# Optimization experiments

Measured on AMD Instinct MI355X. Metric: run time of the kernel, lower is better.

The kernel has to match this reference:

```python
import jax, jax.numpy as jnp
import numpy as np

HEAD_SIZE = 32


def setup_inputs() -> dict:
    key = jax.random.key(0)
    ks = jax.random.split(key, 9)
    B, N, M = 2, 512, 512
    Dq = Dk = Dv = 128
    De = 64
    H, O, OUT = 8, HEAD_SIZE, 128
    s = 0.05  # keep logits tame
    return {
        "query": jax.random.normal(ks[0], (B, N, Dq), jnp.float32),
        "key": jax.random.normal(ks[1], (B, M, Dk), jnp.float32),
        "value": jax.random.normal(ks[2], (B, M, Dv), jnp.float32),
        "edge": jax.random.normal(ks[3], (B, N, M, De), jnp.float32),
        "query_kernel": jax.random.normal(ks[4], (H, Dq, O), jnp.float32) * s,
        "key_kernel": jax.random.normal(ks[5], (H, Dk + De, O), jnp.float32) * s,
        "value_kernel": jax.random.normal(ks[6], (H, Dv, O), jnp.float32) * s,
        "projection_kernel": jax.random.normal(ks[7], (H, O, OUT), jnp.float32) * s,
        "projection_bias": jnp.zeros((OUT,), jnp.float32),
    }


def reference(query, key, value, edge, query_kernel, key_kernel,
              value_kernel, projection_kernel, projection_bias):
    # Edge-conditioned keys: concat broadcast key [B,1,M,Dk] with edge [B,N,M,De]
    B, N, _ = query.shape
    M = key.shape[-2]
    key_rep = jnp.broadcast_to(key[..., None, :, :], (B, N, M, key.shape[-1]))
    key_cat = jnp.concatenate([key_rep, edge], axis=-1)           # [B,N,M,Dk+De]
    k = jnp.einsum('bnmi,hio->bnmho', key_cat, key_kernel)        # [B,N,M,H,O]
    q = jnp.einsum('bni,hio->bnho', query, query_kernel)
    q = q / jnp.sqrt(jnp.asarray(HEAD_SIZE, q.dtype))
    v = jnp.einsum('bmi,hio->bmho', value, value_kernel)
    logits = jnp.einsum('bnho,bnmho->bhnm', q, k)                 # [B,H,N,M]
    attn = jax.nn.softmax(logits, axis=-1)
    mh = jnp.einsum('bhnm,bmho->bnho', attn, v)                   # [B,N,H,O]
    out = jnp.einsum('bnhi,hio->bno', mh, projection_kernel)
    out = out + projection_bias
    return out
```

## Files before the change

kernel.cpp:

```cpp
#include <hip/hip_runtime.h>
#include <hip/hip_bf16.h>

#define B_   2
#define N_   512
#define M_   512
#define D_   128
#define DE_  64
#define H_   8
#define O_   32
#define OUT_ 128
#define DKE_ 192
#define MP_  516

typedef unsigned short u16;
typedef unsigned int   u32;
typedef short bf16x8 __attribute__((ext_vector_type(8)));
typedef float floatx4 __attribute__((ext_vector_type(4)));

__device__ __forceinline__ u32 pk2bf(float a, float b) {
    __hip_bfloat162 h = __float22bfloat162_rn(make_float2(a, b));
    return *reinterpret_cast<u32*>(&h);
}
__device__ __forceinline__ u16 f2bf(float a) {
    __hip_bfloat16 h = __float2bfloat16(a);
    return *reinterpret_cast<u16*>(&h);
}
__device__ __forceinline__ float bf2f(u16 x) {
    return __uint_as_float(((u32)x) << 16);
}
__device__ __forceinline__ bf16x8 cvt8(const float4 a, const float4 b) {
    union { u32 u[4]; bf16x8 v; } r;
    r.u[0] = pk2bf(a.x, a.y); r.u[1] = pk2bf(a.z, a.w);
    r.u[2] = pk2bf(b.x, b.y); r.u[3] = pk2bf(b.z, b.w);
    return r.v;
}

__global__ __launch_bounds__(256) void k_proj(
    const float* __restrict__ query, const float* __restrict__ Wq,
    const float* __restrict__ Wk,
    const float* __restrict__ value, const float* __restrict__ Wv,
    u16* __restrict__ qE, u16* __restrict__ vvT)
{
    const int t = threadIdx.x;
    __shared__ float Xs[8][D_];
    __shared__ float qh[8][H_ * O_];

    if (blockIdx.x < 128) {
        const int r0 = blockIdx.x * 8;
        reinterpret_cast<float4*>(&Xs[0][0])[t] =
            reinterpret_cast<const float4*>(query + (size_t)r0 * D_)[t];
        __syncthreads();
        {
            float acc[8] = {0,0,0,0,0,0,0,0};
            const float* wcol = Wq + (t >> 5) * (D_ * O_) + (t & 31);
            for (int k = 0; k < D_; k += 4) {
                const float w0 = wcol[(k+0) * O_];
                const float w1 = wcol[(k+1) * O_];
                const float w2 = wcol[(k+2) * O_];
                const float w3 = wcol[(k+3) * O_];
#pragma unroll
                for (int r = 0; r < 8; ++r) {
                    const float4 x = *reinterpret_cast<const float4*>(&Xs[r][k]);
                    acc[r] += x.x * w0 + x.y * w1 + x.z * w2 + x.w * w3;
                }
            }
#pragma unroll
            for (int r = 0; r < 8; ++r) qh[r][t] = acc[r] * 0.17677669529663687f;
        }
        __syncthreads();

        for (int s = 0; s < 6; ++s) {
            const int hj = t + 256 * s;
            const int h  = hj / DKE_;
            float w[O_];
#pragma unroll
            for (int i = 0; i < O_ / 4; ++i) {
                const float4 x = reinterpret_cast<const float4*>(Wk + (size_t)hj * O_)[i];
                w[4*i] = x.x; w[4*i+1] = x.y; w[4*i+2] = x.z; w[4*i+3] = x.w;
            }
#pragma unroll
            for (int r = 0; r < 8; ++r) {
                const float* qrow = &qh[r][h * O_];
                float a = 0.f;
#pragma unroll
                for (int i = 0; i < O_ / 4; ++i) {
                    const float4 qx = *reinterpret_cast<const float4*>(qrow + 4*i);
                    a += qx.x * w[4*i] + qx.y * w[4*i+1] + qx.z * w[4*i+2] + qx.w * w[4*i+3];
                }
                qE[(size_t)(r0 + r) * (H_ * DKE_) + hj] = f2bf(a);
            }
        }
    } else {
        const int r0 = (blockIdx.x - 128) * 8;
        reinterpret_cast<float4*>(&Xs[0][0])[t] =
            reinterpret_cast<const float4*>(value + (size_t)r0 * D_)[t];
        __syncthreads();

        float acc[8] = {0,0,0,0,0,0,0,0};
        const float* wcol = Wv + (t >> 5) * (D_ * O_) + (t & 31);
        for (int k = 0; k < D_; k += 4) {
            const float w0 = wcol[(k+0) * O_];
            const float w1 = wcol[(k+1) * O_];
            const float w2 = wcol[(k+2) * O_];
            const float w3 = wcol[(k+3) * O_];
#pragma unroll
            for (int r = 0; r < 8; ++r) {
                const float4 x = *reinterpret_cast<const float4*>(&Xs[r][k]);
                acc[r] += x.x * w0 + x.y * w1 + x.z * w2 + x.w * w3;
            }
        }
        const int bb = r0 >> 9, m0 = r0 & 511;
        union { u32 u[4]; uint4 q; } pk;
        pk.u[0] = pk2bf(acc[0], acc[1]);
        pk.u[1] = pk2bf(acc[2], acc[3]);
        pk.u[2] = pk2bf(acc[4], acc[5]);
        pk.u[3] = pk2bf(acc[6], acc[7]);
        *reinterpret_cast<uint4*>(vvT + (size_t)bb * 256 * M_ + (size_t)t * M_ + m0) = pk.q;
    }
}

__global__ __launch_bounds__(256, 4) void k_attn(
    const float* __restrict__ key, const float* __restrict__ edge,
    const u16* __restrict__ qE, const u16* __restrict__ vvT,
    const float* __restrict__ Wp, const float* __restrict__ bias,
    float* __restrict__ out)
{
    const int idx  = blockIdx.x;
    const int b    = idx >> 9;
    const int t    = threadIdx.x;
    const int lane = t & 63;
    const int wv   = t >> 6;

    __shared__ __attribute__((aligned(16))) float attn_s[H_][MP_];
    __shared__ float mh_s[H_ * O_];
    __shared__ float part_s[2][OUT_];

    const int br = lane & 15;
    const int q  = lane >> 4;

    bf16x8 afr[6];
    if (br < 8) {
        const u16* ab = qE + (size_t)idx * (H_ * DKE_) + br * DKE_;
#pragma unroll
        for (int kk = 0; kk < 6; ++kk)
            afr[kk] = *reinterpret_cast<const bf16x8*>(ab + kk * 32 + q * 8);
    } else {
#pragma unroll
        for (int kk = 0; kk < 6; ++kk) afr[kk] = bf16x8{0,0,0,0,0,0,0,0};
    }

    const float* keyb = key  + (size_t)b   * M_ * D_;
    const float* eb   = edge + (size_t)idx * M_ * DE_;

    for (int it = 0; it < 8; ++it) {
        const int tl = it * 4 + wv;
        const int m  = tl * 16 + br;
        const float* kr = keyb + (size_t)m * D_  + q * 8;
        const float* er = eb   + (size_t)m * DE_ + q * 8;
        float4 kf[8], ef[4];
#pragma unroll
        for (int kk = 0; kk < 4; ++kk) {
            kf[2*kk]   = *reinterpret_cast<const float4*>(kr + kk * 32);
            kf[2*kk+1] = *reinterpret_cast<const float4*>(kr + kk * 32 + 4);
        }
#pragma unroll
        for (int kk = 0; kk < 2; ++kk) {
            ef[2*kk]   = *reinterpret_cast<const float4*>(er + kk * 32);
            ef[2*kk+1] = *reinterpret_cast<const float4*>(er + kk * 32 + 4);
        }
        floatx4 acc = {0.f, 0.f, 0.f, 0.f};
#pragma unroll
        for (int kk = 0; kk < 4; ++kk)
            acc = __builtin_amdgcn_mfma_f32_16x16x32_bf16(afr[kk], cvt8(kf[2*kk], kf[2*kk+1]), acc, 0, 0, 0);
#pragma unroll
        for (int kk = 0; kk < 2; ++kk)
            acc = __builtin_amdgcn_mfma_f32_16x16x32_bf16(afr[4+kk], cvt8(ef[2*kk], ef[2*kk+1]), acc, 0, 0, 0);
        if (q < 2) {
#pragma unroll
            for (int i = 0; i < 4; ++i)
                attn_s[q * 4 + i][tl * 16 + br] = acc[i];
        }
    }
    __syncthreads();

    {
        const int h = t >> 5, ml = t & 31;
        float mx = -3.4e38f;
#pragma unroll 2
        for (int j = 0; j < 16; ++j) mx = fmaxf(mx, attn_s[h][ml + 32 * j]);
#pragma unroll
        for (int mask = 16; mask >= 1; mask >>= 1) mx = fmaxf(mx, __shfl_xor(mx, mask, 64));
        float sum = 0.f;
#pragma unroll 2
        for (int j = 0; j < 16; ++j) {
            const int m = ml + 32 * j;
            const float p = __expf(attn_s[h][m] - mx);
            attn_s[h][m] = p;
            sum += p;
        }
#pragma unroll
        for (int mask = 16; mask >= 1; mask >>= 1) sum += __shfl_xor(sum, mask, 64);
        const float inv = 1.f / sum;
#pragma unroll 2
        for (int j = 0; j < 16; ++j) attn_s[h][ml + 32 * j] *= inv;
    }
    __syncthreads();

    {
        const int hh = t >> 5;
        const u16* vrow = vvT + (size_t)b * 256 * M_ + (size_t)t * M_;
        float a0 = 0.f, a1 = 0.f;
        for (int m0 = 0; m0 < M_; m0 += 8) {
            const bf16x8 v8 = *reinterpret_cast<const bf16x8*>(vrow + m0);
            const float4 w0 = *reinterpret_cast<const float4*>(&attn_s[hh][m0]);
            const float4 w1 = *reinterpret_cast<const float4*>(&attn_s[hh][m0 + 4]);
            a0 += w0.x * bf2f((u16)v8[0]) + w0.y * bf2f((u16)v8[1])
                + w0.z * bf2f((u16)v8[2]) + w0.w * bf2f((u16)v8[3]);
            a1 += w1.x * bf2f((u16)v8[4]) + w1.y * bf2f((u16)v8[5])
                + w1.z * bf2f((u16)v8[6]) + w1.w * bf2f((u16)v8[7]);
        }
        mh_s[t] = a0 + a1;
    }
    __syncthreads();

    {
        const int half = t >> 7;
        const int c = t & 127;
        float acc = 0.f;
        const int j0 = half * 128;
#pragma unroll 8
        for (int jj = 0; jj < 128; ++jj)
            acc += mh_s[j0 + jj] * Wp[(size_t)(j0 + jj) * OUT_ + c];
        part_s[half][c] = acc;
    }
    __syncthreads();
    if (t < OUT_)
        out[(size_t)idx * OUT_ + t] = part_s[0][t] + part_s[1][t] + bias[t];
}

extern "C" void kernel_launch(void* const* d_in, const int* in_sizes, int n_in,
                              void* d_out, int out_size, void* d_ws, size_t ws_size,
                              hipStream_t stream)
{
    const float* query = (const float*)d_in[0];
    const float* key   = (const float*)d_in[1];
    const float* value = (const float*)d_in[2];
    const float* edge  = (const float*)d_in[3];
    const float* Wq    = (const float*)d_in[4];
    const float* Wk    = (const float*)d_in[5];
    const float* Wv    = (const float*)d_in[6];
    const float* Wp    = (const float*)d_in[7];
    const float* bias  = (const float*)d_in[8];
    float* out = (float*)d_out;

    u16* qE_ws = (u16*)d_ws;
    u16* vT_ws = (u16*)((char*)d_ws + (size_t)B_*N_*H_*DKE_*2);

    k_proj<<<256,  256, 0, stream>>>(query, Wq, Wk, value, Wv, qE_ws, vT_ws);
    k_attn<<<1024, 256, 0, stream>>>(key, edge, qE_ws, vT_ws, Wp, bias, out);
}
```

Measured before the change: 276.1 us.

## Pre-convert key to bf16 and double-buffer edge tiles via async LDS loads

Adds blocks to the projection kernel that convert the key tensor to bf16 once, so the attention kernel reads half the key bytes and skips per-block conversion. Edge tiles are now fetched with global_load_lds into a per-wave double buffer, with the next tile prefetched while the current one feeds MFMA, to overlap the dominant edge stream with compute. The extra 32 KB of LDS lowers the occupancy hint from 4 to 3 blocks, and the manual waitcnt encoding must be correct for the data to be valid.

```diff
diff --git a/kernel.cpp b/kernel.cpp
--- a/kernel.cpp
+++ b/kernel.cpp
@@ -16,6 +16,7 @@
 typedef unsigned int   u32;
 typedef short bf16x8 __attribute__((ext_vector_type(8)));
 typedef float floatx4 __attribute__((ext_vector_type(4)));
+typedef u32   u32x4  __attribute__((ext_vector_type(4)));
 
 __device__ __forceinline__ u32 pk2bf(float a, float b) {
     __hip_bfloat162 h = __float22bfloat162_rn(make_float2(a, b));
@@ -28,18 +29,25 @@
 __device__ __forceinline__ float bf2f(u16 x) {
     return __uint_as_float(((u32)x) << 16);
 }
-__device__ __forceinline__ bf16x8 cvt8(const float4 a, const float4 b) {
-    union { u32 u[4]; bf16x8 v; } r;
-    r.u[0] = pk2bf(a.x, a.y); r.u[1] = pk2bf(a.z, a.w);
-    r.u[2] = pk2bf(b.x, b.y); r.u[3] = pk2bf(b.z, b.w);
-    return r.v;
-}
+__device__ __forceinline__ bf16x8 pack8(const float4 a, const float4 b) {
+    u32x4 w;
+    w.x = pk2bf(a.x, a.y); w.y = pk2bf(a.z, a.w);
+    w.z = pk2bf(b.x, b.y); w.w = pk2bf(b.z, b.w);
+    return __builtin_bit_cast(bf16x8, w);
+}
+__device__ __forceinline__ void dma16(const float* g, void* l) {
+    __builtin_amdgcn_global_load_lds(
+        (const __attribute__((address_space(1))) float*)g,
+        (__attribute__((address_space(3))) float*)l, 16, 0, 0);
+}
+#define MEMFENCE() __asm__ volatile("" ::: "memory")
 
 __global__ __launch_bounds__(256) void k_proj(
     const float* __restrict__ query, const float* __restrict__ Wq,
     const float* __restrict__ Wk,
     const float* __restrict__ value, const float* __restrict__ Wv,
-    u16* __restrict__ qE, u16* __restrict__ vvT)
+    const float* __restrict__ key,
+    u16* __restrict__ qE, u16* __restrict__ vvT, u16* __restrict__ keyB)
 {
     const int t = threadIdx.x;
     __shared__ float Xs[8][D_];
@@ -90,7 +98,7 @@
                 qE[(size_t)(r0 + r) * (H_ * DKE_) + hj] = f2bf(a);
             }
         }
-    } else {
+    } else if (blockIdx.x < 256) {
         const int r0 = (blockIdx.x - 128) * 8;
         reinterpret_cast<float4*>(&Xs[0][0])[t] =
             reinterpret_cast<const float4*>(value + (size_t)r0 * D_)[t];
@@ -116,11 +124,23 @@
         pk.u[2] = pk2bf(acc[4], acc[5]);
         pk.u[3] = pk2bf(acc[6], acc[7]);
         *reinterpret_cast<uint4*>(vvT + (size_t)bb * 256 * M_ + (size_t)t * M_ + m0) = pk.q;
-    }
-}
-
-__global__ __launch_bounds__(256, 4) void k_attn(
-    const float* __restrict__ key, const float* __restrict__ edge,
+    } else {
+        const int g = (blockIdx.x - 256) * 256 + t;
+        const float4* src = reinterpret_cast<const float4*>(key);
+#pragma unroll
+        for (int j = 0; j < 8; ++j) {
+            const int i4 = g + j * 4096;
+            const float4 x = src[i4];
+            uint2 p;
+            p.x = pk2bf(x.x, x.y);
+            p.y = pk2bf(x.z, x.w);
+            *reinterpret_cast<uint2*>(keyB + (size_t)i4 * 4) = p;
+        }
+    }
+}
+
+__global__ __launch_bounds__(256, 3) void k_attn(
+    const u16* __restrict__ keyB, const float* __restrict__ edge,
     const u16* __restrict__ qE, const u16* __restrict__ vvT,
     const float* __restrict__ Wp, const float* __restrict__ bias,
     float* __restrict__ out)
@@ -130,14 +150,14 @@
     const int t    = threadIdx.x;
     const int lane = t & 63;
     const int wv   = t >> 6;
-
+    const int br   = lane & 15;
+    const int q    = lane >> 4;
+
+    __shared__ __attribute__((aligned(16))) unsigned char Ebuf[4][2][4096];
     __shared__ __attribute__((aligned(16))) float attn_s[H_][MP_];
     __shared__ float mh_s[H_ * O_];
     __shared__ float part_s[2][OUT_];
 
-    const int br = lane & 15;
-    const int q  = lane >> 4;
-
     bf16x8 afr[6];
     if (br < 8) {
         const u16* ab = qE + (size_t)idx * (H_ * DKE_) + br * DKE_;
@@ -149,37 +169,56 @@
         for (int kk = 0; kk < 6; ++kk) afr[kk] = bf16x8{0,0,0,0,0,0,0,0};
     }
 
-    const float* keyb = key  + (size_t)b   * M_ * D_;
-    const float* eb   = edge + (size_t)idx * M_ * DE_;
-
+    const u16*   kb  = keyB + (size_t)b * M_ * D_;
+    const float* eb  = edge + (size_t)idx * M_ * DE_;
+    const float* ebl = eb + (size_t)(lane & 15) * DE_ + (lane >> 4) * 4;
+
+    {
+        const float* s = ebl + (size_t)(wv * 16) * DE_;
+        char* d = (char*)&Ebuf[wv][0][0];
+#pragma unroll
+        for (int i = 0; i < 4; ++i) dma16(s + i * 16, d + i * 1024);
+    }
+
+    int buf = 0;
+#pragma unroll 1
     for (int it = 0; it < 8; ++it) {
         const int tl = it * 4 + wv;
         const int m  = tl * 16 + br;
-        const float* kr = keyb + (size_t)m * D_  + q * 8;
-        const float* er = eb   + (size_t)m * DE_ + q * 8;
-        float4 kf[8], ef[4];
-#pragma unroll
-        for (int kk = 0; kk < 4; ++kk) {
-            kf[2*kk]   = *reinterpret_cast<const float4*>(kr + kk * 32);
-            kf[2*kk+1] = *reinterpret_cast<const float4*>(kr + kk * 32 + 4);
-        }
+        const u16* kr = kb + (size_t)m * D_ + q * 8;
+        const bf16x8 kf0 = *reinterpret_cast<const bf16x8*>(kr);
+        const bf16x8 kf1 = *reinterpret_cast<const bf16x8*>(kr + 32);
+        const bf16x8 kf2 = *reinterpret_cast<const bf16x8*>(kr + 64);
+        const bf16x8 kf3 = *reinterpret_cast<const bf16x8*>(kr + 96);
+        MEMFENCE();
+        if (it < 7) {
+            const float* s = ebl + (size_t)((tl + 4) * 16) * DE_;
+            char* d = (char*)&Ebuf[wv][buf ^ 1][0];
+#pragma unroll
+            for (int i = 0; i < 4; ++i) dma16(s + i * 16, d + i * 1024);
+        }
+        MEMFENCE();
+        __builtin_amdgcn_s_waitcnt(0x0F74);
+        MEMFENCE();
+
+        floatx4 acc = {0.f, 0.f, 0.f, 0.f};
+        acc = __builtin_amdgcn_mfma_f32_16x16x32_bf16(afr[0], kf0, acc, 0, 0, 0);
+        acc = __builtin_amdgcn_mfma_f32_16x16x32_bf16(afr[1], kf1, acc, 0, 0, 0);
+        acc = __builtin_amdgcn_mfma_f32_16x16x32_bf16(afr[2], kf2, acc, 0, 0, 0);
+        acc = __builtin_amdgcn_mfma_f32_16x16x32_bf16(afr[3], kf3, acc, 0, 0, 0);
+        const char* ebase = (const char*)&Ebuf[wv][buf][0];
 #pragma unroll
         for (int kk = 0; kk < 2; ++kk) {
-            ef[2*kk]   = *reinterpret_cast<const float4*>(er + kk * 32);
-            ef[2*kk+1] = *reinterpret_cast<const float4*>(er + kk * 32 + 4);
-        }
-        floatx4 acc = {0.f, 0.f, 0.f, 0.f};
-#pragma unroll
-        for (int kk = 0; kk < 4; ++kk)
-            acc = __builtin_amdgcn_mfma_f32_16x16x32_bf16(afr[kk], cvt8(kf[2*kk], kf[2*kk+1]), acc, 0, 0, 0);
-#pragma unroll
-        for (int kk = 0; kk < 2; ++kk)
-            acc = __builtin_amdgcn_mfma_f32_16x16x32_bf16(afr[4+kk], cvt8(ef[2*kk], ef[2*kk+1]), acc, 0, 0, 0);
+            const float4 r0 = *reinterpret_cast<const float4*>(ebase + kk * 2048 + q * 512 + br * 16);
+            const float4 r1 = *reinterpret_cast<const float4*>(ebase + kk * 2048 + q * 512 + 256 + br * 16);
+            acc = __builtin_amdgcn_mfma_f32_16x16x32_bf16(afr[4 + kk], pack8(r0, r1), acc, 0, 0, 0);
+        }
         if (q < 2) {
 #pragma unroll
             for (int i = 0; i < 4; ++i)
                 attn_s[q * 4 + i][tl * 16 + br] = acc[i];
         }
+        buf ^= 1;
     }
     __syncthreads();
 
@@ -253,9 +292,11 @@
     const float* bias  = (const float*)d_in[8];
     float* out = (float*)d_out;
 
-    u16* qE_ws = (u16*)d_ws;
-    u16* vT_ws = (u16*)((char*)d_ws + (size_t)B_*N_*H_*DKE_*2);
-
-    k_proj<<<256,  256, 0, stream>>>(query, Wq, Wk, value, Wv, qE_ws, vT_ws);
-    k_attn<<<1024, 256, 0, stream>>>(key, edge, qE_ws, vT_ws, Wp, bias, out);
-}
+    u16* ws    = (u16*)d_ws;
+    u16* qE_ws = ws;
+    u16* vT_ws = ws + 1572864;
+    u16* kB_ws = ws + 1835008;
+
+    k_proj<<<272,  256, 0, stream>>>(query, Wq, Wk, value, Wv, key, qE_ws, vT_ws, kB_ws);
+    k_attn<<<1024, 256, 0, stream>>>(kB_ws, edge, qE_ws, vT_ws, Wp, bias, out);
+}
```

New measurement: 277.0 us. Within noise of the previous version (+0.3%).
